# Optimization experiments

Hardware: AMD Instinct MI355X
Metric: run time of the kernel (lower is better)

## Reference

```python
import jax, jax.numpy as jnp
import numpy as np

N_NODES = 100000
N_EDGES = 6400000
N_FEAT = 128
HIDDEN = 16
N_CLASSES = 16


def gcn_conv(x, edge_index, W, b):
    """PyG GCNConv: y = D^{-1/2}(A+I)D^{-1/2} (x W) + b  (unit edge weights)."""
    n = x.shape[0]
    h = x @ W  # [N, out] dense transform first (PyG order), then sparse aggregate
    loop = jnp.arange(n, dtype=edge_index.dtype)
    src = jnp.concatenate([edge_index[0], loop])  # add self-loops
    dst = jnp.concatenate([edge_index[1], loop])
    deg = jax.ops.segment_sum(jnp.ones_like(dst, dtype=h.dtype), dst, num_segments=n)
    dinv = jnp.where(deg > 0, jax.lax.rsqrt(deg), 0.0)
    norm = dinv[src] * dinv[dst]  # [E+N]
    msgs = norm[:, None] * h[src]  # gather + scale
    out = jax.ops.segment_sum(msgs, dst, num_segments=n)  # scatter-add
    return out + b


def setup_inputs() -> dict:
    key = jax.random.key(0)
    k1, k2, k3, k4 = jax.random.split(key, 4)
    x = jax.random.normal(k1, (N_NODES, N_FEAT), dtype=jnp.float32)
    edge_index = jax.random.randint(k2, (2, N_EDGES), 0, N_NODES, dtype=jnp.int32)
    W1 = jax.random.normal(k3, (N_FEAT, HIDDEN), dtype=jnp.float32) * (1.0 / np.sqrt(N_FEAT))
    b1 = jnp.zeros((HIDDEN,), dtype=jnp.float32)
    W2 = jax.random.normal(k4, (HIDDEN, N_CLASSES), dtype=jnp.float32) * (1.0 / np.sqrt(HIDDEN))
    b2 = jnp.zeros((N_CLASSES,), dtype=jnp.float32)
    return {"x": x, "edge_index": edge_index, "W1": W1, "b1": b1, "W2": W2, "b2": b2}


def reference(x, edge_index, W1, b1, W2, b2):
    h = gcn_conv(x, edge_index, W1, b1)
    h = jax.nn.relu(h)
    # dropout is identity in eval mode (training=False)
    h = gcn_conv(h, edge_index, W2, b2)
    return jax.nn.sigmoid(h)
```

## Files before the change

### kernel.cpp

```cpp
#include <hip/hip_runtime.h>
#include <hip/hip_fp16.h>
#include <math.h>

#define N_NODES 100000
#define N_EDGES 6400000
#define NF 128
#define NH 16
#define NB 128
#define KB 782
#define CAP 9216

#define PT_THREADS 1024
#define PT_EPT 16
#define PT_TILE (PT_THREADS * PT_EPT)
#define PT_BLOCKS ((N_EDGES + PT_TILE - 1) / PT_TILE)
#define PT_WAVES (PT_THREADS / 64)

typedef __attribute__((ext_vector_type(4))) unsigned uv4;

__global__ __launch_bounds__(PT_THREADS) void k_part(const int* __restrict__ src, const int* __restrict__ dst,
                                                     int* __restrict__ bcur, unsigned* __restrict__ part) {
    __shared__ int lcnt[KB];
    __shared__ int lbase[KB];
    __shared__ int cur[KB];
    __shared__ int wsum[PT_WAVES];
    __shared__ int woff[PT_WAVES];
    __shared__ unsigned lsrt[PT_TILE];
    int t = threadIdx.x;
    int e0 = blockIdx.x * PT_TILE;
    int d_reg[PT_EPT];

    for (int i = t; i < KB; i += PT_THREADS) lcnt[i] = 0;
    __syncthreads();
    #pragma unroll
    for (int r = 0; r < PT_EPT; r++) {
        int i = e0 + r * PT_THREADS + t;
        if (i < N_EDGES) {
            d_reg[r] = dst[i];
            atomicAdd(&lcnt[d_reg[r] >> 7], 1);
        } else d_reg[r] = -1;
    }
    __syncthreads();
    int lane_ = t & 63, wv_ = t >> 6;
    int v = (t < KB) ? lcnt[t] : 0;
    int inc = v;
    #pragma unroll
    for (int d = 1; d < 64; d <<= 1) {
        int u = __shfl_up(inc, d, 64);
        if (lane_ >= d) inc += u;
    }
    if (lane_ == 63) wsum[wv_] = inc;
    __syncthreads();
    if (t < PT_WAVES) {
        int s = 0;
        for (int k = 0; k < t; k++) s += wsum[k];
        woff[t] = s;
    }
    __syncthreads();
    if (t < KB) cur[t] = inc - v + woff[wv_];
    for (int b = t; b < KB; b += PT_THREADS) {
        int c = lcnt[b];
        lbase[b] = b * CAP + (c ? atomicAdd(&bcur[b], c) : 0);
    }
    __syncthreads();
    #pragma unroll
    for (int r = 0; r < PT_EPT; r++) {
        int d = d_reg[r];
        if (d >= 0) {
            int i = e0 + r * PT_THREADS + t;
            int p = atomicAdd(&cur[d >> 7], 1);
            lsrt[p] = ((unsigned)src[i] << 7) | (unsigned)(d & (NB - 1));
        }
    }
    __syncthreads();
    int wv = t >> 6, ln = t & 63;
    for (int b = wv; b < KB; b += PT_WAVES) {
        int c = lcnt[b];
        if (!c) continue;
        int gb = lbase[b];
        int lb = cur[b] - c;
        int lim = (b + 1) * CAP - gb;
        int cc = c < lim ? c : lim;
        for (int k = ln; k < cc; k += 64) part[gb + k] = lsrt[lb + k];
    }
}

__global__ __launch_bounds__(512) void k_sort(unsigned* __restrict__ part, const int* __restrict__ bcur,
                                              int* __restrict__ off, int* __restrict__ off_end,
                                              float* __restrict__ dinv) {
    __shared__ int deg[NB];
    __shared__ int sc[NB];
    __shared__ int offl[NB];
    __shared__ int cur[NB];
    __shared__ int lsort[CAP];
    int b = blockIdx.x, t = threadIdx.x;
    int e0 = b * CAP;
    int cnt = bcur[b];
    if (cnt > CAP) cnt = CAP;
    for (int i = t; i < NB; i += 512) deg[i] = 0;
    __syncthreads();
    for (int i = t; i < cnt; i += 512) atomicAdd(&deg[part[e0 + i] & (NB - 1)], 1);
    __syncthreads();
    if (t < NB) sc[t] = deg[t];
    __syncthreads();
    for (int d = 1; d < NB; d <<= 1) {
        int add = (t < NB && t >= d) ? sc[t - d] : 0;
        __syncthreads();
        if (t < NB) sc[t] += add;
        __syncthreads();
    }
    if (t < NB) { int ex = sc[t] - deg[t]; offl[t] = ex; cur[t] = ex; }
    __syncthreads();
    for (int i = t; i < cnt; i += 512) {
        unsigned u = part[e0 + i];
        int r = atomicAdd(&cur[u & (NB - 1)], 1);
        lsort[r] = (int)(u >> 7);
    }
    __syncthreads();
    for (int i = t; i < cnt; i += 512) part[e0 + i] = (unsigned)lsort[i];
    if (t < NB) {
        int n = b * NB + t;
        if (n < N_NODES) {
            off[n] = e0 + offl[t];
            off_end[n] = e0 + offl[t] + deg[t];
            dinv[n] = rsqrtf((float)(deg[t] + 1));
        }
    }
}

__global__ __launch_bounds__(256) void k_gemm1(const float* __restrict__ x, const float* __restrict__ W1,
                                               const float* __restrict__ dinv, __half* __restrict__ g1) {
    __shared__ float Ws[NF * NH];
    for (int i = threadIdx.x; i < NF * NH; i += 256) Ws[i] = W1[i];
    __syncthreads();
    int gid = blockIdx.x * 256 + threadIdx.x;
    int n = gid >> 4, j = gid & 15;
    if (n >= N_NODES) return;
    const float4* xr = (const float4*)(x + (size_t)n * NF);
    float acc = 0.f;
    #pragma unroll
    for (int k4 = 0; k4 < NF / 4; k4++) {
        float4 v = xr[k4];
        acc += v.x * Ws[(k4 * 4 + 0) * NH + j];
        acc += v.y * Ws[(k4 * 4 + 1) * NH + j];
        acc += v.z * Ws[(k4 * 4 + 2) * NH + j];
        acc += v.w * Ws[(k4 * 4 + 3) * NH + j];
    }
    g1[(size_t)n * NH + j] = __float2half(dinv[n] * acc);
}

__device__ __forceinline__ __half2 shx(__half2 x, int m) {
    union { __half2 h; int i; } u;
    u.h = x;
    u.i = __shfl_xor(u.i, m, 64);
    return u.h;
}

__device__ __forceinline__ uv4 make_srd(const void* p, unsigned bytes) {
    union { const void* q; unsigned u[2]; } a; a.q = p;
    uv4 r;
    r.x = a.u[0];
    r.y = a.u[1];
    r.z = bytes;
    r.w = 0x00020000u;
    return r;
}

template <int LAYER>
__global__ __launch_bounds__(256) void k_agg(const __half* __restrict__ g, const int* __restrict__ off,
                                             const int* __restrict__ off_end,
                                             const unsigned* __restrict__ sorted,
                                             const float* __restrict__ dinv,
                                             const float* __restrict__ bias, const float* __restrict__ W2,
                                             void* __restrict__ outp) {
    __shared__ __align__(16) unsigned redu[4][8];
    __shared__ float redf[4][NH];
    __shared__ __align__(16) float W2T[16 * 20];
    int t = threadIdx.x;
    if (LAYER == 1) {
        int j = t >> 4, k = t & 15;
        W2T[j * 20 + k] = W2[k * 16 + j];
        __syncthreads();
    }
    int w = t >> 6, lane = t & 63;
    int n = blockIdx.x * 4 + w;
    int slot = lane & 31, c = lane >> 5;
    int o0 = off[n], o1 = off_end[n];

    const uv4 srd = make_srd(g, (unsigned)(N_NODES * NH * sizeof(__half)));
    unsigned cofs = (unsigned)(c << 4);

    int j = lane & 15;
    float dn = dinv[n];
    float selfj = __half2float(g[(size_t)n * NH + j]);

    union HV { uv4 q; __half2 h[4]; };
    __half2 a0 = __half2(0.f, 0.f), a1 = a0, a2 = a0, a3 = a0;
    for (int eb = o0; eb < o1; eb += 128) {
        int e1 = eb + slot;
        unsigned s1 = sorted[e1];
        unsigned s2 = sorted[e1 + 32];
        unsigned s3 = sorted[e1 + 64];
        unsigned s4 = sorted[e1 + 96];
        if (e1      >= o1) s1 = 1u << 26;
        if (e1 + 32 >= o1) s2 = 1u << 26;
        if (e1 + 64 >= o1) s3 = 1u << 26;
        if (e1 + 96 >= o1) s4 = 1u << 26;
        unsigned f1 = (s1 << 5) + cofs;
        unsigned f2 = (s2 << 5) + cofs;
        unsigned f3 = (s3 << 5) + cofs;
        unsigned f4 = (s4 << 5) + cofs;
        HV v1, v2, v3, v4;
        asm volatile("buffer_load_dwordx4 %0, %1, %2, 0 offen" : "=v"(v1.q) : "v"(f1), "s"(srd));
        asm volatile("buffer_load_dwordx4 %0, %1, %2, 0 offen" : "=v"(v2.q) : "v"(f2), "s"(srd));
        asm volatile("buffer_load_dwordx4 %0, %1, %2, 0 offen" : "=v"(v3.q) : "v"(f3), "s"(srd));
        asm volatile("buffer_load_dwordx4 %0, %1, %2, 0 offen" : "=v"(v4.q) : "v"(f4), "s"(srd));
        asm volatile("s_waitcnt vmcnt(0)" ::: "memory");
        __builtin_amdgcn_sched_barrier(0);
        a0 = __hadd2(a0, __hadd2(__hadd2(v1.h[0], v2.h[0]), __hadd2(v3.h[0], v4.h[0])));
        a1 = __hadd2(a1, __hadd2(__hadd2(v1.h[1], v2.h[1]), __hadd2(v3.h[1], v4.h[1])));
        a2 = __hadd2(a2, __hadd2(__hadd2(v1.h[2], v2.h[2]), __hadd2(v3.h[2], v4.h[2])));
        a3 = __hadd2(a3, __hadd2(__hadd2(v1.h[3], v2.h[3]), __hadd2(v3.h[3], v4.h[3])));
    }
    #pragma unroll
    for (int m = 1; m <= 16; m <<= 1) {
        a0 = __hadd2(a0, shx(a0, m));
        a1 = __hadd2(a1, shx(a1, m));
        a2 = __hadd2(a2, shx(a2, m));
        a3 = __hadd2(a3, shx(a3, m));
    }
    if (slot == 0) {
        union { uint4 q; __half2 h[4]; } p;
        p.h[0] = a0; p.h[1] = a1; p.h[2] = a2; p.h[3] = a3;
        *(uint4*)&redu[w][c * 4] = p.q;
    }
    union { unsigned u; __half2 h; } pick;
    pick.u = redu[w][((j >> 3) << 2) + ((j & 7) >> 1)];
    float sumj = __half2float((j & 1) ? __high2half(pick.h) : __low2half(pick.h));
    if (LAYER == 1) {
        if (lane < NH) {
            redf[w][j] = fmaxf(fmaf(dn, sumj + selfj, bias[j]), 0.f);
            float4 r0 = *(const float4*)&redf[w][0];
            float4 r1 = *(const float4*)&redf[w][4];
            float4 r2 = *(const float4*)&redf[w][8];
            float4 r3 = *(const float4*)&redf[w][12];
            const float* wr = &W2T[j * 20];
            float4 w0 = *(const float4*)&wr[0];
            float4 w1 = *(const float4*)&wr[4];
            float4 w2 = *(const float4*)&wr[8];
            float4 w3 = *(const float4*)&wr[12];
            float h = r0.x * w0.x + r0.y * w0.y + r0.z * w0.z + r0.w * w0.w
                    + r1.x * w1.x + r1.y * w1.y + r1.z * w1.z + r1.w * w1.w
                    + r2.x * w2.x + r2.y * w2.y + r2.z * w2.z + r2.w * w2.w
                    + r3.x * w3.x + r3.y * w3.y + r3.z * w3.z + r3.w * w3.w;
            ((__half*)outp)[(size_t)n * NH + j] = __float2half(dn * h);
        }
    } else {
        if (lane < NH) {
            float z = fmaf(dn, sumj + selfj, bias[j]);
            ((float*)outp)[(size_t)n * NH + j] = 1.f / (1.f + __expf(-z));
        }
    }
}

extern "C" void kernel_launch(void* const* d_in, const int* in_sizes, int n_in,
                              void* d_out, int out_size, void* d_ws, size_t ws_size,
                              hipStream_t stream) {
    const float* x  = (const float*)d_in[0];
    const int* eidx = (const int*)d_in[1];
    const float* W1 = (const float*)d_in[2];
    const float* b1 = (const float*)d_in[3];
    const float* W2 = (const float*)d_in[4];
    const float* b2 = (const float*)d_in[5];
    const int* src = eidx;
    const int* dst = eidx + N_EDGES;
    float* out = (float*)d_out;

    char* ws = (char*)d_ws;
    size_t o = 0;
    auto alloc = [&](size_t bytes) { size_t r = o; o = (o + bytes + 255) & ~(size_t)255; return r; };
    int*      bcur    = (int*)     (ws + alloc(sizeof(int) * KB));
    unsigned* part    = (unsigned*)(ws + alloc(sizeof(unsigned) * ((size_t)KB * CAP + 512)));
    int*      off     = (int*)     (ws + alloc(sizeof(int) * N_NODES));
    int*      off_end = (int*)     (ws + alloc(sizeof(int) * N_NODES));
    float*    dinv    = (float*)   (ws + alloc(sizeof(float) * N_NODES));
    __half*   g1      = (__half*)  (ws + alloc(sizeof(__half) * N_NODES * NH));
    __half*   g2      = (__half*)  (ws + alloc(sizeof(__half) * N_NODES * NH));
    (void)ws_size; (void)n_in; (void)in_sizes; (void)out_size;

    hipMemsetAsync(bcur, 0, sizeof(int) * KB, stream);

    k_part<<<PT_BLOCKS, PT_THREADS, 0, stream>>>(src, dst, bcur, part);
    k_sort<<<KB, 512, 0, stream>>>(part, bcur, off, off_end, dinv);

    k_gemm1<<<(N_NODES * NH + 255) / 256, 256, 0, stream>>>(x, W1, dinv, g1);

    k_agg<1><<<N_NODES / 4, 256, 0, stream>>>(g1, off, off_end, part, dinv, b1, W2, g2);
    k_agg<2><<<N_NODES / 4, 256, 0, stream>>>(g2, off, off_end, part, dinv, b2, nullptr, out);
}
```

Baseline: 189.4 us.

## Replace inline buffer loads with guarded plain gathers, larger blocks and deeper unroll

The aggregation kernel drops its hand-written buffer_load asm, the explicit vmcnt(0) wait and the sentinel-index trick. It now uses guarded plain global uint4 gathers with nontemporal index loads, unrolled six-wide per iteration. Blocks grow from 4 to 16 nodes (1024 threads) with a launch-bounds occupancy hint, which amortises per-block setup and may raise occupancy. Branching per load could serialise the gathers or stop the compiler from batching them, and the larger blocks add tail imbalance.

```diff
diff --git a/kernel.cpp b/kernel.cpp
--- a/kernel.cpp
+++ b/kernel.cpp
@@ -16,7 +16,8 @@
 #define PT_BLOCKS ((N_EDGES + PT_TILE - 1) / PT_TILE)
 #define PT_WAVES (PT_THREADS / 64)
 
-typedef __attribute__((ext_vector_type(4))) unsigned uv4;
+#define AG_THREADS 1024
+#define AG_NODES 16
 
 __global__ __launch_bounds__(PT_THREADS) void k_part(const int* __restrict__ src, const int* __restrict__ dst,
                                                      int* __restrict__ bcur, unsigned* __restrict__ part) {
@@ -156,71 +157,74 @@
     return u.h;
 }
 
-__device__ __forceinline__ uv4 make_srd(const void* p, unsigned bytes) {
-    union { const void* q; unsigned u[2]; } a; a.q = p;
-    uv4 r;
-    r.x = a.u[0];
-    r.y = a.u[1];
-    r.z = bytes;
-    r.w = 0x00020000u;
-    return r;
-}
-
 template <int LAYER>
-__global__ __launch_bounds__(256) void k_agg(const __half* __restrict__ g, const int* __restrict__ off,
-                                             const int* __restrict__ off_end,
-                                             const unsigned* __restrict__ sorted,
-                                             const float* __restrict__ dinv,
-                                             const float* __restrict__ bias, const float* __restrict__ W2,
-                                             void* __restrict__ outp) {
-    __shared__ __align__(16) unsigned redu[4][8];
-    __shared__ float redf[4][NH];
+__global__ __launch_bounds__(AG_THREADS, 8) void k_agg(const __half* __restrict__ g, const int* __restrict__ off,
+                                                       const int* __restrict__ off_end,
+                                                       const unsigned* __restrict__ sorted,
+                                                       const float* __restrict__ dinv,
+                                                       const float* __restrict__ bias, const float* __restrict__ W2,
+                                                       void* __restrict__ outp) {
+    __shared__ __align__(16) unsigned redu[AG_NODES][8];
+    __shared__ float redf[AG_NODES][NH];
     __shared__ __align__(16) float W2T[16 * 20];
     int t = threadIdx.x;
     if (LAYER == 1) {
-        int j = t >> 4, k = t & 15;
-        W2T[j * 20 + k] = W2[k * 16 + j];
+        if (t < 256) {
+            int j = t >> 4, k = t & 15;
+            W2T[j * 20 + k] = W2[k * 16 + j];
+        }
         __syncthreads();
     }
     int w = t >> 6, lane = t & 63;
-    int n = blockIdx.x * 4 + w;
+    int n = blockIdx.x * AG_NODES + w;
     int slot = lane & 31, c = lane >> 5;
     int o0 = off[n], o1 = off_end[n];
-
-    const uv4 srd = make_srd(g, (unsigned)(N_NODES * NH * sizeof(__half)));
-    unsigned cofs = (unsigned)(c << 4);
+    const char* gbase = (const char*)g + (c << 4);
 
     int j = lane & 15;
     float dn = dinv[n];
     float selfj = __half2float(g[(size_t)n * NH + j]);
 
-    union HV { uv4 q; __half2 h[4]; };
+    union HV { uint4 q; __half2 h[4]; };
     __half2 a0 = __half2(0.f, 0.f), a1 = a0, a2 = a0, a3 = a0;
-    for (int eb = o0; eb < o1; eb += 128) {
+    for (int eb = o0; eb < o1; eb += 192) {
         int e1 = eb + slot;
-        unsigned s1 = sorted[e1];
-        unsigned s2 = sorted[e1 + 32];
-        unsigned s3 = sorted[e1 + 64];
-        unsigned s4 = sorted[e1 + 96];
-        if (e1      >= o1) s1 = 1u << 26;
-        if (e1 + 32 >= o1) s2 = 1u << 26;
-        if (e1 + 64 >= o1) s3 = 1u << 26;
-        if (e1 + 96 >= o1) s4 = 1u << 26;
-        unsigned f1 = (s1 << 5) + cofs;
-        unsigned f2 = (s2 << 5) + cofs;
-        unsigned f3 = (s3 << 5) + cofs;
-        unsigned f4 = (s4 << 5) + cofs;
-        HV v1, v2, v3, v4;
-        asm volatile("buffer_load_dwordx4 %0, %1, %2, 0 offen" : "=v"(v1.q) : "v"(f1), "s"(srd));
-        asm volatile("buffer_load_dwordx4 %0, %1, %2, 0 offen" : "=v"(v2.q) : "v"(f2), "s"(srd));
-        asm volatile("buffer_load_dwordx4 %0, %1, %2, 0 offen" : "=v"(v3.q) : "v"(f3), "s"(srd));
-        asm volatile("buffer_load_dwordx4 %0, %1, %2, 0 offen" : "=v"(v4.q) : "v"(f4), "s"(srd));
-        asm volatile("s_waitcnt vmcnt(0)" ::: "memory");
-        __builtin_amdgcn_sched_barrier(0);
-        a0 = __hadd2(a0, __hadd2(__hadd2(v1.h[0], v2.h[0]), __hadd2(v3.h[0], v4.h[0])));
-        a1 = __hadd2(a1, __hadd2(__hadd2(v1.h[1], v2.h[1]), __hadd2(v3.h[1], v4.h[1])));
-        a2 = __hadd2(a2, __hadd2(__hadd2(v1.h[2], v2.h[2]), __hadd2(v3.h[2], v4.h[2])));
-        a3 = __hadd2(a3, __hadd2(__hadd2(v1.h[3], v2.h[3]), __hadd2(v3.h[3], v4.h[3])));
+        if (e1 < o1) {
+            unsigned s = __builtin_nontemporal_load(&sorted[e1]);
+            HV v; v.q = *(const uint4*)(gbase + ((size_t)s << 5));
+            a0 = __hadd2(a0, v.h[0]); a1 = __hadd2(a1, v.h[1]);
+            a2 = __hadd2(a2, v.h[2]); a3 = __hadd2(a3, v.h[3]);
+        }
+        if (e1 + 32 < o1) {
+            unsigned s = __builtin_nontemporal_load(&sorted[e1 + 32]);
+            HV v; v.q = *(const uint4*)(gbase + ((size_t)s << 5));
+            a0 = __hadd2(a0, v.h[0]); a1 = __hadd2(a1, v.h[1]);
+            a2 = __hadd2(a2, v.h[2]); a3 = __hadd2(a3, v.h[3]);
+        }
+        if (e1 + 64 < o1) {
+            unsigned s = __builtin_nontemporal_load(&sorted[e1 + 64]);
+            HV v; v.q = *(const uint4*)(gbase + ((size_t)s << 5));
+            a0 = __hadd2(a0, v.h[0]); a1 = __hadd2(a1, v.h[1]);
+            a2 = __hadd2(a2, v.h[2]); a3 = __hadd2(a3, v.h[3]);
+        }
+        if (e1 + 96 < o1) {
+            unsigned s = __builtin_nontemporal_load(&sorted[e1 + 96]);
+            HV v; v.q = *(const uint4*)(gbase + ((size_t)s << 5));
+            a0 = __hadd2(a0, v.h[0]); a1 = __hadd2(a1, v.h[1]);
+            a2 = __hadd2(a2, v.h[2]); a3 = __hadd2(a3, v.h[3]);
+        }
+        if (e1 + 128 < o1) {
+            unsigned s = __builtin_nontemporal_load(&sorted[e1 + 128]);
+            HV v; v.q = *(const uint4*)(gbase + ((size_t)s << 5));
+            a0 = __hadd2(a0, v.h[0]); a1 = __hadd2(a1, v.h[1]);
+            a2 = __hadd2(a2, v.h[2]); a3 = __hadd2(a3, v.h[3]);
+        }
+        if (e1 + 160 < o1) {
+            unsigned s = __builtin_nontemporal_load(&sorted[e1 + 160]);
+            HV v; v.q = *(const uint4*)(gbase + ((size_t)s << 5));
+            a0 = __hadd2(a0, v.h[0]); a1 = __hadd2(a1, v.h[1]);
+            a2 = __hadd2(a2, v.h[2]); a3 = __hadd2(a3, v.h[3]);
+        }
     }
     #pragma unroll
     for (int m = 1; m <= 16; m <<= 1) {
@@ -295,6 +299,6 @@
 
     k_gemm1<<<(N_NODES * NH + 255) / 256, 256, 0, stream>>>(x, W1, dinv, g1);
 
-    k_agg<1><<<N_NODES / 4, 256, 0, stream>>>(g1, off, off_end, part, dinv, b1, W2, g2);
-    k_agg<2><<<N_NODES / 4, 256, 0, stream>>>(g2, off, off_end, part, dinv, b2, nullptr, out);
-}
+    k_agg<1><<<N_NODES / AG_NODES, AG_THREADS, 0, stream>>>(g1, off, off_end, part, dinv, b1, W2, g2);
+    k_agg<2><<<N_NODES / AG_NODES, AG_THREADS, 0, stream>>>(g2, off, off_end, part, dinv, b2, nullptr, out);
+}
```

Measured after the change: 213.9 us. 13.0% more time.
